# Kernel optimization log

Hardware: AMD Instinct MI355X
Metric: run time of the kernel (lower is better)

The kernel has to match this reference:

```python
import jax, jax.numpy as jnp
import numpy as np

EPS = 1e-5

def _conv2d(x, w, b, pad):
    y = jax.lax.conv_general_dilated(x, w, (1, 1), [(pad, pad), (pad, pad)],
                                     dimension_numbers=('NCHW', 'OIHW', 'NCHW'))
    return y + b[None, :, None, None]

def _layernorm2d(x, g, beta):
    # channel-wise LayerNorm per spatial location (LayerNorm2d)
    mu = jnp.mean(x, axis=1, keepdims=True)
    var = jnp.var(x, axis=1, keepdims=True)
    return (x - mu) * jax.lax.rsqrt(var + EPS) * g[None, :, None, None] + beta[None, :, None, None]

def _deform_conv2d(x, offset, w, b, pad):
    # torchvision deform_conv2d semantics (stride 1, dilation 1, 1 group, no mask)
    # x: [B,C,H,W]; offset: [B,2*K*K,H,W] with (dy,dx) per kernel tap; w: [O,C,K,K]
    B, C, H, W = x.shape
    K = w.shape[-1]
    off = offset.reshape(B, K * K, 2, H, W)
    by = jnp.arange(H, dtype=x.dtype)[:, None]   # [H,1]
    bx = jnp.arange(W, dtype=x.dtype)[None, :]   # [1,W]

    def sample(im, py, px):
        # im [C,H,W], py/px [H,W] -> bilinear sample with zero padding outside
        y0 = jnp.floor(py); x0 = jnp.floor(px)
        wy = py - y0; wx = px - x0
        y0i = y0.astype(jnp.int32); x0i = x0.astype(jnp.int32)
        def g(yi, xi):
            valid = (yi >= 0) & (yi < H) & (xi >= 0) & (xi < W)
            v = im[:, jnp.clip(yi, 0, H - 1), jnp.clip(xi, 0, W - 1)]
            return v * valid.astype(im.dtype)
        v00 = g(y0i, x0i);     v01 = g(y0i, x0i + 1)
        v10 = g(y0i + 1, x0i); v11 = g(y0i + 1, x0i + 1)
        return (v00 * (1 - wy) * (1 - wx) + v01 * (1 - wy) * wx
                + v10 * wy * (1 - wx) + v11 * wy * wx)

    vsample = jax.vmap(sample)
    out = jnp.zeros((B, w.shape[0], H, W), dtype=x.dtype)
    for k in range(K * K):  # small fixed tap loop (<=49)
        ki, kj = k // K, k % K
        py = by + (ki - pad) + off[:, k, 0]  # [B,H,W]
        px = bx + (kj - pad) + off[:, k, 1]
        s = vsample(x, py, px)               # [B,C,H,W]
        out = out + jnp.einsum('bchw,oc->bohw', s, w[:, :, ki, kj])
    return out + b[None, :, None, None]


def setup_inputs() -> dict:
    key = jax.random.key(0)
    ks = jax.random.split(key, 12)
    B, C, H, W = 4, 64, 192, 192
    s = 0.02
    inp = {
        'x': jax.random.normal(ks[0], (B, C, H, W), jnp.float32),
        'ln_w': jnp.ones((C,), jnp.float32),
        'ln_b': jnp.zeros((C,), jnp.float32),
        'w_in': jax.random.normal(ks[1], (2 * C, C), jnp.float32) * s,
        'b_in': jnp.zeros((2 * C,), jnp.float32),
        'w_out': jax.random.normal(ks[2], (C, C), jnp.float32) * s,
        'b_out': jnp.zeros((C,), jnp.float32),
        'dw1': jax.random.normal(ks[3], (C, C, 7, 7), jnp.float32) * s,
        'db1': jnp.zeros((C,), jnp.float32),
        'dw2': jax.random.normal(ks[4], (C, C, 5, 5), jnp.float32) * s,
        'db2': jnp.zeros((C,), jnp.float32),
        'dw3': jax.random.normal(ks[5], (C, C, 3, 3), jnp.float32) * s,
        'db3': jnp.zeros((C,), jnp.float32),
        'ow1': jax.random.normal(ks[6], (2 * 7 * 7, C, 5, 5), jnp.float32) * s,
        'ob1': jnp.zeros((2 * 7 * 7,), jnp.float32),
        'ow2': jax.random.normal(ks[7], (2 * 5 * 5, C, 5, 5), jnp.float32) * s,
        'ob2': jnp.zeros((2 * 5 * 5,), jnp.float32),
        'ow3': jax.random.normal(ks[8], (2 * 3 * 3, C, 3, 3), jnp.float32) * s,
        'ob3': jnp.zeros((2 * 3 * 3,), jnp.float32),
    }
    return inp


def reference(x, ln_w, ln_b, w_in, b_in, w_out, b_out,
              dw1, db1, dw2, db2, dw3, db3,
              ow1, ob1, ow2, ob2, ow3, ob3):
    tmp = x
    h = _layernorm2d(x, ln_w, ln_b)
    h = jnp.einsum('bchw,oc->bohw', h, w_in) + b_in[None, :, None, None]  # 1x1 conv_in
    C = x.shape[1]
    x1, x2 = h[:, :C], h[:, C:]
    off = _conv2d(x1, ow1, ob1, 2)
    x1 = _deform_conv2d(x1, off, dw1, db1, 3)
    off = _conv2d(x1, ow2, ob2, 2)
    x1 = _deform_conv2d(x1, off, dw2, db2, 2)
    off = _conv2d(x1, ow3, ob3, 1)
    x1 = _deform_conv2d(x1, off, dw3, db3, 1)
    h = x1 + x2
    h = jnp.einsum('bchw,oc->bohw', h, w_out) + b_out[None, :, None, None]  # 1x1 conv_out
    return h + tmp
```

## Files before the change

kernel.cpp:

```cpp
#include <hip/hip_runtime.h>

#define HH 192
#define WID 192
#define HW (HH*WID)
#define CB 64
#define BB 4
#define NPOS (BB*HW)

typedef __attribute__((ext_vector_type(8))) _Float16 half8v;
typedef __attribute__((ext_vector_type(4))) _Float16 half4v;
typedef __attribute__((ext_vector_type(4))) float f32x4;
typedef __attribute__((ext_vector_type(16))) float f32x16;

static __device__ inline half8v splat8(_Float16 x) {
    half8v v = {x, x, x, x, x, x, x, x};
    return v;
}


template<int KK, int CO, int OP>
__global__ void k_wth(const float* __restrict__ w, _Float16* __restrict__ wt)
{
    int idx = blockIdx.x * 256 + threadIdx.x;
    constexpr int TOT = KK * OP * 64;
    if (idx >= TOT) return;
    int k  = idx / (OP * 64);
    int r  = idx % (OP * 64);
    int cs = r / (OP * 8);
    int r2 = r % (OP * 8);
    int o  = r2 / 8;
    int j  = r2 % 8;
    int c  = cs * 8 + j;
    float v = (o < CO) ? w[((size_t)o * 64 + c) * KK + k] : 0.f;
    wt[idx] = (_Float16)v;
}

__global__ __launch_bounds__(256) void k_lnconv_mfma(
    const float* __restrict__ x, const float* __restrict__ g, const float* __restrict__ be,
    const _Float16* __restrict__ wt_in, const float* __restrict__ b_in,
    _Float16* __restrict__ x1, _Float16* __restrict__ x2)
{
    int p0  = blockIdx.x * 128;
    int b   = p0 / HW;
    int hwb = p0 % HW;

    int lane = threadIdx.x & 63;
    int wave = threadIdx.x >> 6;
    int l31  = lane & 31;
    int h    = lane >> 5;
    int pos  = hwb + wave * 32 + l31;

    const float* xp = x + (size_t)b * CB * HW + pos;

    float v[32];
    float sum = 0.f, sumsq = 0.f;
#pragma unroll
    for (int m = 0; m < 4; m++)
#pragma unroll
        for (int j = 0; j < 8; j++) {
            float t = xp[(size_t)(m * 16 + h * 8 + j) * HW];
            v[m * 8 + j] = t; sum += t; sumsq += t * t;
        }
    sum   += __shfl_xor(sum, 32);
    sumsq += __shfl_xor(sumsq, 32);
    float mu  = sum * (1.f / 64.f);
    float var = sumsq * (1.f / 64.f) - mu * mu;
    float inv = rsqrtf(var + 1e-5f);

    half8v bf[4];
#pragma unroll
    for (int m = 0; m < 4; m++)
#pragma unroll
        for (int j = 0; j < 8; j++) {
            int c = m * 16 + h * 8 + j;
            bf[m][j] = (_Float16)((v[m * 8 + j] - mu) * inv * g[c] + be[c]);
        }

    f32x16 acc[4];
#pragma unroll
    for (int tI = 0; tI < 4; tI++)
#pragma unroll
        for (int r = 0; r < 16; r++) acc[tI][r] = 0.f;

    const half8v* wbase = (const half8v*)wt_in;
#pragma unroll
    for (int m = 0; m < 4; m++) {
        int cs = m * 2 + h;
        const half8v* wp = wbase + (size_t)cs * 128;
#pragma unroll
        for (int tI = 0; tI < 4; tI++) {
            half8v a = wp[tI * 32 + l31];
            acc[tI] = __builtin_amdgcn_mfma_f32_32x32x16_f16(a, bf[m], acc[tI], 0, 0, 0);
        }
    }

    _Float16* o1 = x1 + (size_t)b * HW * 64 + (size_t)pos * 8;
    _Float16* o2 = x2 + (size_t)b * HW * 64 + (size_t)pos * 8;
#pragma unroll
    for (int tI = 0; tI < 4; tI++) {
        _Float16* ob = (tI < 2) ? o1 : o2;
        int obase = (tI & 1) * 32;
#pragma unroll
        for (int gidx = 0; gidx < 4; gidx++) {
            int o = obase + gidx * 8 + 4 * h;
            float4 bb = *(const float4*)&b_in[tI * 32 + gidx * 8 + 4 * h];
            half4v r;
            r[0] = (_Float16)(acc[tI][gidx * 4 + 0] + bb.x);
            r[1] = (_Float16)(acc[tI][gidx * 4 + 1] + bb.y);
            r[2] = (_Float16)(acc[tI][gidx * 4 + 2] + bb.z);
            r[3] = (_Float16)(acc[tI][gidx * 4 + 3] + bb.w);
            *(half4v*)&ob[(size_t)(o >> 3) * HW * 8 + (o & 7)] = r;
        }
    }
}

template<int K, int PAD, int HALO>
__global__ __launch_bounds__(256) void k_sconv(
    const _Float16* __restrict__ xin, const float* __restrict__ offp,
    const _Float16* __restrict__ wtb, const float* __restrict__ bias,
    _Float16* __restrict__ outp)
{
    constexpr int KK = K * K;
    constexpr int RB = 16 + 2 * HALO;
    constexpr int WB = 8  + 2 * HALO;

    __shared__ half8v sm[RB * WB * 8];

    int bi  = blockIdx.x;
    int b   = bi / 288;
    int tt  = bi % 288;
    int by0 = (tt / 24) * 16;
    int bx0 = (tt % 24) * 8;
    int ry0 = by0 - HALO;
    int rx0 = bx0 - HALO;

    const _Float16* xb  = xin + (size_t)b * HW * 64;

    {
        _Float16* smlin = (_Float16*)sm;
        constexpr int CH = RB * WB * 8;
        for (int i0 = 0; i0 < CH; i0 += 256) {
            int i     = i0 + (int)threadIdx.x;
            int wbse  = i0 + ((int)threadIdx.x & 192);
            if (i < CH) {
                int pix = i >> 3;
                int ts  = i & 7;
                int pl  = ts ^ (pix & 7);
                int r   = pix / WB;
                int cc  = pix - r * WB;
                int yr  = min(max(ry0 + r,  0), HH - 1);
                int xc  = min(max(rx0 + cc, 0), WID - 1);
                const _Float16* src = xb + ((size_t)pl * HW + (size_t)(yr * WID + xc)) * 8;
                __builtin_amdgcn_global_load_lds(src, &smlin[(size_t)wbse * 8], 16, 0, 0);
            }
        }
    }
    __syncthreads();

    int t    = threadIdx.x;
    int lane = t & 63;
    int wave = t >> 6;
    int l31  = lane & 31;
    int h    = lane >> 5;
    int prow = l31 >> 3;
    int pcol = l31 & 7;

    int yt = by0 + wave * 4 + prow;
    int xt = bx0 + pcol;
    int gp = b * HW + yt * WID + xt;

    const half8v* wbase = (const half8v*)wtb;

    f32x16 acc0 = {0.f,0.f,0.f,0.f,0.f,0.f,0.f,0.f,0.f,0.f,0.f,0.f,0.f,0.f,0.f,0.f};
    f32x16 acc1 = {0.f,0.f,0.f,0.f,0.f,0.f,0.f,0.f,0.f,0.f,0.f,0.f,0.f,0.f,0.f,0.f};

    const float2* offj = (const float2*)offp + gp;
    float2 offc = offj[0];

    int ki = 0, kj = 0;
    for (int k = 0; k < KK; k++) {
        float2 offn = offj[(size_t)(k + 1) * NPOS];

        half8v a0[4], a1[4];
#pragma unroll
        for (int m = 0; m < 4; m++) {
            int cs = m * 2 + h;
            const half8v* wp = wbase + ((size_t)k * 8 + cs) * 64;
            a0[m] = wp[l31];
            a1[m] = wp[32 + l31];
        }

        float py = (float)(yt + ki - PAD) + offc.x;
        float px = (float)(xt + kj - PAD) + offc.y;
        float fy = floorf(py), fx = floorf(px);
        float wy = py - fy, wx = px - fx;
        int iy0 = (int)fy, ix0 = (int)fx;
        int iy1 = iy0 + 1, ix1 = ix0 + 1;
        float m00 = (iy0 >= 0 && iy0 < HH && ix0 >= 0 && ix0 < WID) ? 1.f : 0.f;
        float m01 = (iy0 >= 0 && iy0 < HH && ix1 >= 0 && ix1 < WID) ? 1.f : 0.f;
        float m10 = (iy1 >= 0 && iy1 < HH && ix0 >= 0 && ix0 < WID) ? 1.f : 0.f;
        float m11 = (iy1 >= 0 && iy1 < HH && ix1 >= 0 && ix1 < WID) ? 1.f : 0.f;
        half8v w00v = splat8((_Float16)((1.f - wy) * (1.f - wx) * m00));
        half8v w01v = splat8((_Float16)((1.f - wy) * wx * m01));
        half8v w10v = splat8((_Float16)(wy * (1.f - wx) * m10));
        half8v w11v = splat8((_Float16)(wy * wx * m11));

        bool fast = (iy0 >= ry0) && (iy1 <= ry0 + RB - 1) &&
                    (ix0 >= rx0) && (ix1 <= rx0 + WB - 1);

        if (__builtin_expect(fast, 1)) {
            int p00 = (iy0 - ry0) * WB + (ix0 - rx0);
            int p01 = p00 + 1, p10 = p00 + WB, p11 = p00 + WB + 1;
            int s00 = p00 & 7, s01 = p01 & 7, s10 = p10 & 7, s11 = p11 & 7;
#pragma unroll
            for (int m = 0; m < 4; m++) {
                int cs = m * 2 + h;
                half8v c00 = sm[p00 * 8 + (cs ^ s00)];
                half8v c01 = sm[p01 * 8 + (cs ^ s01)];
                half8v c10 = sm[p10 * 8 + (cs ^ s10)];
                half8v c11 = sm[p11 * 8 + (cs ^ s11)];
                half8v bf = c00 * w00v + c01 * w01v + c10 * w10v + c11 * w11v;
                acc0 = __builtin_amdgcn_mfma_f32_32x32x16_f16(a0[m], bf, acc0, 0, 0, 0);
                acc1 = __builtin_amdgcn_mfma_f32_32x32x16_f16(a1[m], bf, acc1, 0, 0, 0);
            }
        } else {
            int cy0 = min(max(iy0, 0), HH - 1), cy1 = min(max(iy1, 0), HH - 1);
            int cx0 = min(max(ix0, 0), WID - 1), cx1 = min(max(ix1, 0), WID - 1);
            size_t i00 = (size_t)(cy0 * WID + cx0) * 8, i01 = (size_t)(cy0 * WID + cx1) * 8;
            size_t i10 = (size_t)(cy1 * WID + cx0) * 8, i11 = (size_t)(cy1 * WID + cx1) * 8;
#pragma unroll
            for (int m = 0; m < 4; m++) {
                const _Float16* xq = xb + (size_t)(m * 2 + h) * HW * 8;
                half8v c00 = *(const half8v*)(xq + i00);
                half8v c01 = *(const half8v*)(xq + i01);
                half8v c10 = *(const half8v*)(xq + i10);
                half8v c11 = *(const half8v*)(xq + i11);
                half8v bf = c00 * w00v + c01 * w01v + c10 * w10v + c11 * w11v;
                acc0 = __builtin_amdgcn_mfma_f32_32x32x16_f16(a0[m], bf, acc0, 0, 0, 0);
                acc1 = __builtin_amdgcn_mfma_f32_32x32x16_f16(a1[m], bf, acc1, 0, 0, 0);
            }
        }

        offc = offn;
        kj++;
        if (kj == K) { kj = 0; ki++; }
    }

    int hwp = yt * WID + xt;
    _Float16* ob = outp + (size_t)b * HW * 64 + (size_t)hwp * 8 + 4 * h;
#pragma unroll
    for (int g = 0; g < 4; g++) {
        float4 bb0 = *(const float4*)&bias[g * 8 + 4 * h];
        half4v r0;
        r0[0] = (_Float16)(acc0[g * 4 + 0] + bb0.x);
        r0[1] = (_Float16)(acc0[g * 4 + 1] + bb0.y);
        r0[2] = (_Float16)(acc0[g * 4 + 2] + bb0.z);
        r0[3] = (_Float16)(acc0[g * 4 + 3] + bb0.w);
        *(half4v*)&ob[(size_t)g * HW * 8] = r0;
        float4 bb1 = *(const float4*)&bias[32 + g * 8 + 4 * h];
        half4v r1;
        r1[0] = (_Float16)(acc1[g * 4 + 0] + bb1.x);
        r1[1] = (_Float16)(acc1[g * 4 + 1] + bb1.y);
        r1[2] = (_Float16)(acc1[g * 4 + 2] + bb1.z);
        r1[3] = (_Float16)(acc1[g * 4 + 3] + bb1.w);
        *(half4v*)&ob[(size_t)(4 + g) * HW * 8] = r1;
    }
}

template<int K, int PAD, int NTILE, int CO>
__global__ __launch_bounds__(256) void k_soconv(
    const _Float16* __restrict__ xin,
    const _Float16* __restrict__ wtb, const float* __restrict__ bias,
    float* __restrict__ outf)
{
    constexpr int KK = K * K;
    constexpr int KTAP = CO / 2;
    constexpr int HALO = PAD;
    constexpr int RB = 16 + 2 * HALO;
    constexpr int WB = 8  + 2 * HALO;
    constexpr int OP = NTILE * 32;

    __shared__ half8v sm[RB * WB * 8];

    int bi  = blockIdx.x;
    int b   = bi / 288;
    int tt  = bi % 288;
    int by0 = (tt / 24) * 16;
    int bx0 = (tt % 24) * 8;
    int ry0 = by0 - HALO;
    int rx0 = bx0 - HALO;

    const _Float16* xb = xin + (size_t)b * HW * 64;

    {
        _Float16* smlin = (_Float16*)sm;
        constexpr int CH = RB * WB * 8;
        for (int i0 = 0; i0 < CH; i0 += 256) {
            int i    = i0 + (int)threadIdx.x;
            int wbse = i0 + ((int)threadIdx.x & 192);
            if (i < CH) {
                int pix = i >> 3;
                int ts  = i & 7;
                int pl  = ts ^ (pix & 7);
                int r   = pix / WB;
                int cc  = pix - r * WB;
                int yr  = ry0 + r;
                int xc  = rx0 + cc;
                bool ok = (yr >= 0 && yr < HH && xc >= 0 && xc < WID);
                if (ok) {
                    const _Float16* src = xb + ((size_t)pl * HW + (size_t)(yr * WID + xc)) * 8;
                    __builtin_amdgcn_global_load_lds(src, &smlin[(size_t)wbse * 8], 16, 0, 0);
                } else {
                    *(half8v*)&smlin[(size_t)i * 8] = splat8((_Float16)0.f);
                }
            }
        }
    }
    __syncthreads();

    int lane = threadIdx.x & 63;
    int wave = threadIdx.x >> 6;
    int l31  = lane & 31;
    int h    = lane >> 5;
    int prow = l31 >> 3;
    int pcol = l31 & 7;

    int yt = by0 + wave * 4 + prow;
    int xt = bx0 + pcol;
    int gp = b * HW + yt * WID + xt;

    const half8v* wbase = (const half8v*)wtb;

    f32x16 acc[NTILE];
#pragma unroll
    for (int tI = 0; tI < NTILE; tI++)
#pragma unroll
        for (int r = 0; r < 16; r++) acc[tI][r] = 0.f;

    int ki = 0, kj = 0;
    for (int k = 0; k < KK; k++) {
        int rr  = (yt + ki - PAD) - ry0;
        int ccx = (xt + kj - PAD) - rx0;
        int pix = rr * WB + ccx;
        int s   = pix & 7;

#pragma unroll
        for (int m = 0; m < 4; m++) {
            int cs = m * 2 + h;
            half8v bf = sm[pix * 8 + (cs ^ s)];
            const half8v* wp = wbase + ((size_t)k * 8 + cs) * OP;
#pragma unroll
            for (int tI = 0; tI < NTILE; tI++) {
                half8v a = wp[tI * 32 + l31];
                acc[tI] = __builtin_amdgcn_mfma_f32_32x32x16_f16(a, bf, acc[tI], 0, 0, 0);
            }
        }

        kj++;
        if (kj == K) { kj = 0; ki++; }
    }

#pragma unroll
    for (int tI = 0; tI < NTILE; tI++) {
#pragma unroll
        for (int g = 0; g < 4; g++) {
            int base = tI * 32 + 8 * g + 4 * h;
#pragma unroll
            for (int pr = 0; pr < 2; pr++) {
                int o  = base + 2 * pr;
                int t0 = o >> 1;
                if (t0 < KTAP) {
                    float2 r;
                    r.x = acc[tI][g * 4 + 2 * pr]     + bias[o];
                    r.y = acc[tI][g * 4 + 2 * pr + 1] + bias[o + 1];
                    *(float2*)&outf[((size_t)t0 * NPOS + gp) * 2] = r;
                }
            }
        }
    }
}

__global__ __launch_bounds__(256) void k_merge_mfma(
    const _Float16* __restrict__ x1f, const _Float16* __restrict__ x2,
    const float* __restrict__ xin, const _Float16* __restrict__ wt_out,
    const float* __restrict__ b_out, float* __restrict__ out)
{
    int p0  = blockIdx.x * 128;
    int b   = p0 / HW;
    int hwb = p0 % HW;

    int lane = threadIdx.x & 63;
    int wave = threadIdx.x >> 6;
    int l31  = lane & 31;
    int h    = lane >> 5;
    int pos  = hwb + wave * 32 + l31;

    const _Float16* a1 = x1f + (size_t)b * HW * 64 + (size_t)pos * 8;
    const _Float16* a2 = x2  + (size_t)b * HW * 64 + (size_t)pos * 8;

    half8v bf[4];
#pragma unroll
    for (int m = 0; m < 4; m++) {
        int cs = m * 2 + h;
        half8v u1 = *(const half8v*)&a1[(size_t)cs * HW * 8];
        half8v u2 = *(const half8v*)&a2[(size_t)cs * HW * 8];
        bf[m] = u1 + u2;
    }

    f32x16 acc[2];
#pragma unroll
    for (int tI = 0; tI < 2; tI++)
#pragma unroll
        for (int r = 0; r < 16; r++) acc[tI][r] = 0.f;

    const half8v* wbase = (const half8v*)wt_out;
#pragma unroll
    for (int m = 0; m < 4; m++) {
        int cs = m * 2 + h;
        const half8v* wp = wbase + (size_t)cs * 64;
#pragma unroll
        for (int tI = 0; tI < 2; tI++) {
            half8v a = wp[tI * 32 + l31];
            acc[tI] = __builtin_amdgcn_mfma_f32_32x32x16_f16(a, bf[m], acc[tI], 0, 0, 0);
        }
    }

    size_t base = (size_t)b * CB * HW + pos;
#pragma unroll
    for (int tI = 0; tI < 2; tI++) {
#pragma unroll
        for (int gidx = 0; gidx < 4; gidx++) {
            int o0 = tI * 32 + gidx * 8 + 4 * h;
#pragma unroll
            for (int i = 0; i < 4; i++) {
                int o = o0 + i;
                out[base + (size_t)o * HW] =
                    acc[tI][gidx * 4 + i] + b_out[o] + xin[base + (size_t)o * HW];
            }
        }
    }
}

extern "C" void kernel_launch(void* const* d_in, const int* in_sizes, int n_in,
                              void* d_out, int out_size, void* d_ws, size_t ws_size,
                              hipStream_t stream)
{
    const float* x     = (const float*)d_in[0];
    const float* ln_w  = (const float*)d_in[1];
    const float* ln_b  = (const float*)d_in[2];
    const float* w_in  = (const float*)d_in[3];
    const float* b_in  = (const float*)d_in[4];
    const float* w_out = (const float*)d_in[5];
    const float* b_out = (const float*)d_in[6];
    const float* dw1   = (const float*)d_in[7];
    const float* db1   = (const float*)d_in[8];
    const float* dw2   = (const float*)d_in[9];
    const float* db2   = (const float*)d_in[10];
    const float* dw3   = (const float*)d_in[11];
    const float* db3   = (const float*)d_in[12];
    const float* ow1   = (const float*)d_in[13];
    const float* ob1   = (const float*)d_in[14];
    const float* ow2   = (const float*)d_in[15];
    const float* ob2   = (const float*)d_in[16];
    const float* ow3   = (const float*)d_in[17];
    const float* ob3   = (const float*)d_in[18];

    _Float16* x1a = (_Float16*)d_ws;
    _Float16* x1b = x1a + (size_t)NPOS * 64;
    _Float16* x2  = x1b + (size_t)NPOS * 64;
    float* off = (float*)(x2 + (size_t)NPOS * 64);
    _Float16* wtd1 = (_Float16*)(off + (size_t)NPOS * 100);
    _Float16* wtd2 = wtd1 + 49 * 64 * 64;
    _Float16* wtd3 = wtd2 + 25 * 64 * 64;
    _Float16* wto1 = wtd3 +  9 * 64 * 64;
    _Float16* wto2 = wto1 + 25 * 128 * 64;
    _Float16* wto3 = wto2 + 25 * 64 * 64;
    _Float16* wtin = wto3 +  9 * 32 * 64;
    _Float16* wtou = wtin + 128 * 64;

    k_wth<49, 64,  64><<<784, 256, 0, stream>>>(dw1, wtd1);
    k_wth<25, 64,  64><<<400, 256, 0, stream>>>(dw2, wtd2);
    k_wth< 9, 64,  64><<<144, 256, 0, stream>>>(dw3, wtd3);
    k_wth<25, 98, 128><<<800, 256, 0, stream>>>(ow1, wto1);
    k_wth<25, 50,  64><<<400, 256, 0, stream>>>(ow2, wto2);
    k_wth< 9, 18,  32><<< 72, 256, 0, stream>>>(ow3, wto3);
    k_wth< 1, 128, 128><<<32, 256, 0, stream>>>(w_in, wtin);
    k_wth< 1, 64,  64><<<16, 256, 0, stream>>>(w_out, wtou);

    k_lnconv_mfma<<<NPOS / 128, 256, 0, stream>>>(x, ln_w, ln_b, wtin, b_in, x1a, x2);

    k_soconv<5, 2, 4, 98><<<1152, 256, 0, stream>>>(x1a, wto1, ob1, off);
    k_sconv<7, 3, 4><<<1152, 256, 0, stream>>>(x1a, off, wtd1, db1, x1b);
    k_soconv<5, 2, 2, 50><<<1152, 256, 0, stream>>>(x1b, wto2, ob2, off);
    k_sconv<5, 2, 3><<<1152, 256, 0, stream>>>(x1b, off, wtd2, db2, x1a);
    k_soconv<3, 1, 1, 18><<<1152, 256, 0, stream>>>(x1a, wto3, ob3, off);
    k_sconv<3, 1, 2><<<1152, 256, 0, stream>>>(x1a, off, wtd3, db3, x1b);

    k_merge_mfma<<<NPOS / 128, 256, 0, stream>>>(x1b, x2, x, wtou, b_out, (float*)d_out);
}
```

Before: 581.8 us.

## Split offset-conv output channel tiles across waves instead of per-wave loops

The offset-prediction convolution previously had each wave compute all NTILE output-channel tiles for its own 4-row pixel group, loading one LDS fragment and NTILE weight fragments per step. Now waves are split by output-channel tile (ct) and pixel group, and each wave loops over CT pixel groups. This cuts per-wave global weight loads and gives waves more independent accumulators that share one weight fragment. The trade is more LDS reads per MFMA, and if the wave count does not divide evenly the row coverage assumption (4 waves, CT groups) could change.

```diff
diff --git a/kernel.cpp b/kernel.cpp
--- a/kernel.cpp
+++ b/kernel.cpp
@@ -267,7 +267,7 @@
     }
 }
 
-template<int K, int PAD, int NTILE, int CO>
+template<int K, int PAD, int CT, int CO>
 __global__ __launch_bounds__(256) void k_soconv(
     const _Float16* __restrict__ xin,
     const _Float16* __restrict__ wtb, const float* __restrict__ bias,
@@ -278,7 +278,7 @@
     constexpr int HALO = PAD;
     constexpr int RB = 16 + 2 * HALO;
     constexpr int WB = 8  + 2 * HALO;
-    constexpr int OP = NTILE * 32;
+    constexpr int OP = CT * 32;
 
     __shared__ half8v sm[RB * WB * 8];
 
@@ -325,34 +325,43 @@
     int prow = l31 >> 3;
     int pcol = l31 & 7;
 
-    int yt = by0 + wave * 4 + prow;
+    int ct = wave % CT;
+    int pp = wave / CT;
+
     int xt = bx0 + pcol;
-    int gp = b * HW + yt * WID + xt;
+    int yt[CT], gp[CT];
+#pragma unroll
+    for (int q = 0; q < CT; q++) {
+        int g = pp * CT + q;
+        yt[q] = by0 + g * 4 + prow;
+        gp[q] = b * HW + yt[q] * WID + xt;
+    }
 
     const half8v* wbase = (const half8v*)wtb;
 
-    f32x16 acc[NTILE];
-#pragma unroll
-    for (int tI = 0; tI < NTILE; tI++)
-#pragma unroll
-        for (int r = 0; r < 16; r++) acc[tI][r] = 0.f;
+    f32x16 acc[CT];
+#pragma unroll
+    for (int q = 0; q < CT; q++)
+#pragma unroll
+        for (int r = 0; r < 16; r++) acc[q][r] = 0.f;
 
     int ki = 0, kj = 0;
     for (int k = 0; k < KK; k++) {
-        int rr  = (yt + ki - PAD) - ry0;
         int ccx = (xt + kj - PAD) - rx0;
-        int pix = rr * WB + ccx;
-        int s   = pix & 7;
+        int pix[CT];
+#pragma unroll
+        for (int q = 0; q < CT; q++)
+            pix[q] = ((yt[q] + ki - PAD) - ry0) * WB + ccx;
 
 #pragma unroll
         for (int m = 0; m < 4; m++) {
             int cs = m * 2 + h;
-            half8v bf = sm[pix * 8 + (cs ^ s)];
             const half8v* wp = wbase + ((size_t)k * 8 + cs) * OP;
-#pragma unroll
-            for (int tI = 0; tI < NTILE; tI++) {
-                half8v a = wp[tI * 32 + l31];
-                acc[tI] = __builtin_amdgcn_mfma_f32_32x32x16_f16(a, bf, acc[tI], 0, 0, 0);
+            half8v a = wp[ct * 32 + l31];
+#pragma unroll
+            for (int q = 0; q < CT; q++) {
+                half8v bf = sm[pix[q] * 8 + (cs ^ (pix[q] & 7))];
+                acc[q] = __builtin_amdgcn_mfma_f32_32x32x16_f16(a, bf, acc[q], 0, 0, 0);
             }
         }
 
@@ -361,19 +370,19 @@
     }
 
 #pragma unroll
-    for (int tI = 0; tI < NTILE; tI++) {
-#pragma unroll
-        for (int g = 0; g < 4; g++) {
-            int base = tI * 32 + 8 * g + 4 * h;
+    for (int q = 0; q < CT; q++) {
+#pragma unroll
+        for (int gi = 0; gi < 4; gi++) {
+            int obase = ct * 32 + 8 * gi + 4 * h;
 #pragma unroll
             for (int pr = 0; pr < 2; pr++) {
-                int o  = base + 2 * pr;
+                int o  = obase + 2 * pr;
                 int t0 = o >> 1;
                 if (t0 < KTAP) {
                     float2 r;
-                    r.x = acc[tI][g * 4 + 2 * pr]     + bias[o];
-                    r.y = acc[tI][g * 4 + 2 * pr + 1] + bias[o + 1];
-                    *(float2*)&outf[((size_t)t0 * NPOS + gp) * 2] = r;
+                    r.x = acc[q][gi * 4 + 2 * pr]     + bias[o];
+                    r.y = acc[q][gi * 4 + 2 * pr + 1] + bias[o + 1];
+                    *(float2*)&outf[((size_t)t0 * NPOS + gp[q]) * 2] = r;
                 }
             }
         }
```

Result: faster. 530.9 us (-8.7%).
